# Kernel tuning notes

Measured on AMD Instinct MI355X. Metric: run time of the kernel, lower is better.

## Reference

```python
import jax, jax.numpy as jnp
from jax import lax
import numpy as np

D_MODEL = 1024
D_STATE = 16
D_CONV = 4
EXPAND = 2
D_INNER = EXPAND * D_MODEL
IN_DIM = 256
OUT_DIM = 256
B = 2
T = 1024
LN_EPS = 1e-5


def setup_inputs() -> dict:
    key = jax.random.key(0)
    ks = jax.random.split(key, 10)
    s = lambda k, shape: (jax.random.normal(k, shape, dtype=jnp.float32) * 0.02)
    inp = {}
    inp["x"] = jax.random.normal(ks[0], (B, T, IN_DIM), dtype=jnp.float32)
    inp["hidden_state"] = jnp.zeros((B, D_INNER, D_STATE), dtype=jnp.float32)
    # wrapper input projection (Linear with bias)
    inp["W_in_wrap"] = s(ks[1], (IN_DIM, D_MODEL))
    inp["b_in_wrap"] = jnp.zeros((D_MODEL,), jnp.float32)
    # LayerNorm
    inp["ln_gamma"] = jnp.ones((D_MODEL,), jnp.float32)
    inp["ln_beta"] = jnp.zeros((D_MODEL,), jnp.float32)
    # Mamba block params
    inp["W_in"] = s(ks[2], (D_MODEL, 2 * D_INNER))          # in_proj, no bias
    inp["conv_w"] = s(ks[3], (D_INNER, 1, D_CONV))           # depthwise conv kernel (O,I/G,K)
    inp["conv_b"] = jnp.zeros((D_INNER,), jnp.float32)
    inp["W_x"] = s(ks[4], (D_INNER, 2 * D_STATE + D_INNER))  # x_proj, no bias
    inp["W_dt"] = s(ks[5], (D_INNER, D_INNER))
    inp["b_dt"] = jnp.zeros((D_INNER,), jnp.float32)
    A = jnp.tile(jnp.arange(1, D_STATE + 1, dtype=jnp.float32)[None, :], (D_INNER, 1))
    inp["A_log"] = jnp.log(A)
    inp["D_skip"] = jnp.ones((D_INNER,), jnp.float32)
    inp["W_out"] = s(ks[6], (D_INNER, D_MODEL))              # out_proj, no bias
    # wrapper output projection (Linear with bias)
    inp["W_out_wrap"] = s(ks[7], (D_MODEL, OUT_DIM))
    inp["b_out_wrap"] = jnp.zeros((OUT_DIM,), jnp.float32)
    return inp


def _silu(x):
    return x * jax.nn.sigmoid(x)


def _layernorm(x, gamma, beta):
    mu = jnp.mean(x, axis=-1, keepdims=True)
    var = jnp.mean(jnp.square(x - mu), axis=-1, keepdims=True)
    return (x - mu) * lax.rsqrt(var + LN_EPS) * gamma + beta


def _mamba_forward(x, hidden_state, W_in_wrap, b_in_wrap, ln_gamma, ln_beta,
                   W_in, conv_w, conv_b, W_x, W_dt, b_dt, A_log, D_skip,
                   W_out, W_out_wrap, b_out_wrap):
    # wrapper: input projection + layernorm
    h = x @ W_in_wrap + b_in_wrap            # [B,T,d_model]
    h = _layernorm(h, ln_gamma, ln_beta)

    # Mamba block
    xz = h @ W_in                             # [B,T,2*d_inner]
    x_branch, z = jnp.split(xz, 2, axis=-1)

    # causal depthwise conv1d (torch pads both sides by d_conv-1, slices to seq_len == left-pad only)
    xc = lax.conv_general_dilated(
        x_branch.transpose(0, 2, 1),          # [B, d_inner, T]
        conv_w,                               # [d_inner, 1, K]
        window_strides=(1,),
        padding=[(D_CONV - 1, 0)],
        feature_group_count=D_INNER,
        dimension_numbers=('NCH', 'OIH', 'NCH'))
    xc = xc + conv_b[None, :, None]
    u = _silu(xc.transpose(0, 2, 1))          # [B,T,d_inner]

    proj = u @ W_x                            # [B,T,2n+d_inner]
    B_in = proj[..., :D_STATE]                # [B,T,n]
    C_in = proj[..., D_STATE:2 * D_STATE]     # [B,T,n]
    dt = jax.nn.softplus(proj[..., 2 * D_STATE:] @ W_dt + b_dt)  # [B,T,d_inner]

    A = -jnp.exp(A_log)                       # [d_inner,n]
    dA = jnp.exp(dt[..., None] * A)                              # [B,T,d,n]
    dBu = dt[..., None] * B_in[:, :, None, :] * u[..., None]     # [B,T,d,n]

    def step(h_c, inputs):
        dA_t, dBu_t, C_t = inputs             # [B,d,n],[B,d,n],[B,n]
        h_c = dA_t * h_c + dBu_t
        y_t = jnp.einsum('bdn,bn->bd', h_c, C_t)
        return h_c, y_t

    hT, ys = lax.scan(step, hidden_state,
                      (dA.transpose(1, 0, 2, 3), dBu.transpose(1, 0, 2, 3), C_in.transpose(1, 0, 2)))
    y = ys.transpose(1, 0, 2)                 # [B,T,d_inner]
    y = y + u * D_skip
    y = y * _silu(z)
    out = (y @ W_out) @ W_out_wrap + b_out_wrap
    return out, hT


def reference(x, hidden_state, W_in_wrap, b_in_wrap, ln_gamma, ln_beta,
              W_in, conv_w, conv_b, W_x, W_dt, b_dt, A_log, D_skip,
              W_out, W_out_wrap, b_out_wrap):
    return _mamba_forward(x, hidden_state, W_in_wrap, b_in_wrap, ln_gamma, ln_beta,
                          W_in, conv_w, conv_b, W_x, W_dt, b_dt, A_log, D_skip,
                          W_out, W_out_wrap, b_out_wrap)
```

## Files before the change

kernel.cpp:

```cpp
#include <hip/hip_runtime.h>
#include <cstddef>
#include <cstdint>

#define D_MODEL 1024
#define D_STATE 16
#define D_CONV 4
#define D_INNER 2048
#define IN_DIM 256
#define OUT_DIM 256
#define BATCH 2
#define SEQ 1024
#define NTOK (BATCH*SEQ)
#define PROJ_N (2*D_STATE + D_INNER)
#define CHUNK 64
#define NCHUNK (SEQ/CHUNK)

typedef __attribute__((ext_vector_type(8))) short bf16x8;
typedef __attribute__((ext_vector_type(4))) float f32x4;

__device__ __forceinline__ float siluf(float x){ return x / (1.f + __expf(-x)); }

__device__ __forceinline__ unsigned short f2bf(float f) {
  uint32_t x = __float_as_uint(f);
  uint32_t r = x + 0x7fffu + ((x >> 16) & 1u);
  return (unsigned short)(r >> 16);
}
__device__ __forceinline__ float bf2f(unsigned short u) {
  return __uint_as_float(((uint32_t)u) << 16);
}

template<int k, typename T, int N>
__device__ __forceinline__ T (&pick4(T (&a)[N], T (&b)[N], T (&c)[N], T (&d)[N]))[N] {
  if constexpr (k == 0) return a; else if constexpr (k == 1) return b;
  else if constexpr (k == 2) return c; else return d;
}

__device__ __forceinline__ void tc_tile(float (*tile)[33], const float* __restrict__ in,
                                        unsigned short* __restrict__ out,
                                        int R, int C, int tcx, int tcy, int tid)
{
  const int bc = tcx * 32, br = tcy * 32;
  const int tx = tid & 31, ty = tid >> 5;
  #pragma unroll
  for (int i = 0; i < 4; ++i) {
    int r = ty + i*8;
    tile[r][tx] = in[(size_t)(br + r)*C + bc + tx];
  }
  __syncthreads();
  const int otx = tid & 7, oty = tid >> 3;
  ushort4 v;
  v.x = f2bf(tile[otx*4+0][oty]);
  v.y = f2bf(tile[otx*4+1][oty]);
  v.z = f2bf(tile[otx*4+2][oty]);
  v.w = f2bf(tile[otx*4+3][oty]);
  *(ushort4*)&out[(size_t)(bc + oty)*R + br + otx*4] = v;
}

__global__ __launch_bounds__(256)
void prep_k(const float* __restrict__ x, const float* __restrict__ Wiw,
            const float* __restrict__ Win, const float* __restrict__ Wx,
            const float* __restrict__ Wdt, const float* __restrict__ Wout,
            const float* __restrict__ Wwr,
            unsigned short* __restrict__ xb16, unsigned short* __restrict__ WiwT,
            unsigned short* __restrict__ WinT, unsigned short* __restrict__ WxT,
            unsigned short* __restrict__ WdtT, unsigned short* __restrict__ Wob,
            unsigned short* __restrict__ WwrT)
{
  __shared__ float tile[32][33];
  const int tid = threadIdx.x;
  int id = blockIdx.x;
  if (id < 4096)  { tc_tile(tile, Win,  WinT,  1024, 4096, id % 128, id / 128, tid); return; }
  id -= 4096;
  if (id < 4160)  { tc_tile(tile, Wx,   WxT,   2048, 2080, id % 65,  id / 65,  tid); return; }
  id -= 4160;
  if (id < 4096)  { tc_tile(tile, Wdt,  WdtT,  2048, 2048, id % 64,  id / 64,  tid); return; }
  id -= 4096;
  if (id < 2048) {
    int i = id * 256 + tid;
    float4 v = ((const float4*)Wout)[i];
    ushort4 o;
    o.x = f2bf(v.x); o.y = f2bf(v.y); o.z = f2bf(v.z); o.w = f2bf(v.w);
    ((ushort4*)Wob)[i] = o;
    return;
  }
  id -= 2048;
  if (id < 256)   { tc_tile(tile, Wwr,  WwrT,  1024, 256,  id % 8,   id / 8,   tid); return; }
  id -= 256;
  if (id < 256)   { tc_tile(tile, Wiw,  WiwT,  256,  1024, id % 32,  id / 32,  tid); return; }
  id -= 256;
  if (id < 512) {
    int i = id * 256 + tid;
    float4 v = ((const float4*)x)[i];
    ushort4 o;
    o.x = f2bf(v.x); o.y = f2bf(v.y); o.z = f2bf(v.z); o.w = f2bf(v.w);
    ((ushort4*)xb16)[i] = o;
    return;
  }
  id -= 512;
  {
    unsigned short* p = WxT + (size_t)(2080 + id) * 2048 + tid * 8;
    ushort4 z = {0,0,0,0};
    *(ushort4*)p = z; *(ushort4*)(p + 4) = z;
  }
}

template<int BM, int BN, int MODE>
__global__ __launch_bounds__(256)
void gemm_bf16(const unsigned short* __restrict__ A, const unsigned short* __restrict__ B,
               int M, int N, int K, int lda, int ldb,
               const float* __restrict__ bias,
               void* __restrict__ out0, void* __restrict__ out1)
{
  constexpr int FM = BM / 32;
  constexpr int FN = BN / 32;
  constexpr int ROWS = BM + BN;
  constexpr int GR = ROWS / 64;
  __shared__ __align__(1024) unsigned short S[2][ROWS*32];

  const int tid = threadIdx.x;
  const int lane = tid & 63, w = tid >> 6;
  const int row0 = blockIdx.y * BM, col0 = blockIdx.x * BN;
  const int wr = (w >> 1) * (BM/2), wc = (w & 1) * (BN/2);
  const int l15 = lane & 15, lg4 = lane >> 4;

  size_t zoff = 0;
  if constexpr (MODE == 5) {
    A += (size_t)blockIdx.z * (size_t)K;
    B += (size_t)blockIdx.z * (size_t)K;
    zoff = (size_t)blockIdx.z * (size_t)(gridDim.y * BM) * (size_t)N;
  }

  int afo[FM], bfo[FN];
  #pragma unroll
  for (int fi = 0; fi < FM; ++fi) {
    const int r = wr + fi*16 + l15;
    afo[fi] = r*32 + (lg4 ^ ((r >> 1) & 3))*8;
  }
  #pragma unroll
  for (int fj = 0; fj < FN; ++fj) {
    const int r = wc + fj*16 + l15;
    bfo[fj] = (BM + r)*32 + (lg4 ^ ((r >> 1) & 3))*8;
  }

  const unsigned short* src[GR];
  int ldso[GR];
  #pragma unroll
  for (int i = 0; i < GR; ++i) {
    const int g = tid + i*256;
    const int row = g >> 2, q = g & 3;
    ldso[i] = row*32 + (q ^ ((row >> 1) & 3))*8;
    src[i] = (row < BM) ? A + (size_t)(row0 + row) * lda + q*8
                        : B + (size_t)(col0 + row - BM) * ldb + q*8;
  }

  f32x4 acc[FM][FN];
  #pragma unroll
  for (int i=0;i<FM;i++)
    #pragma unroll
    for (int j=0;j<FN;j++) acc[i][j] = (f32x4){0.f,0.f,0.f,0.f};

  const int NT = K >> 5;
  bf16x8 g0[GR], g1[GR], g2[GR], g3[GR];

  auto loadg = [&](bf16x8 (&g)[GR]) {
    #pragma unroll
    for (int i = 0; i < GR; ++i) { g[i] = *(const bf16x8*)src[i]; src[i] += 32; }
  };

  loadg(g0); loadg(g1); loadg(g2); loadg(g3);
  #pragma unroll
  for (int i = 0; i < GR; ++i) *(bf16x8*)(&S[0][ldso[i]]) = g0[i];
  asm volatile("s_waitcnt lgkmcnt(0)" ::: "memory");
  __builtin_amdgcn_s_barrier();
  asm volatile("" ::: "memory");

#define STEP(I) do {                                                          \
    const int j = base + (I);                                                 \
    if (j < NT) {                                                             \
      bf16x8 af[FM], bfv[FN];                                                 \
      _Pragma("unroll")                                                       \
      for (int fi = 0; fi < FM; ++fi)                                         \
        af[fi] = *(const bf16x8*)&S[(I)&1][afo[fi]];                          \
      _Pragma("unroll")                                                       \
      for (int fj = 0; fj < FN; ++fj)                                         \
        bfv[fj] = *(const bf16x8*)&S[(I)&1][bfo[fj]];                         \
      if (j + 4 < NT) loadg(pick4<(I)&3>(g0, g1, g2, g3));                    \
      _Pragma("unroll")                                                       \
      for (int fi = 0; fi < FM; ++fi)                                         \
        _Pragma("unroll")                                                     \
        for (int fj = 0; fj < FN; ++fj)                                       \
          acc[fi][fj] = __builtin_amdgcn_mfma_f32_16x16x32_bf16(              \
              af[fi], bfv[fj], acc[fi][fj], 0, 0, 0);                         \
      if (j + 1 < NT) {                                                       \
        bf16x8 (&gw)[GR] = pick4<((I)+1)&3>(g0, g1, g2, g3);                  \
        _Pragma("unroll")                                                     \
        for (int i = 0; i < GR; ++i)                                          \
          *(bf16x8*)(&S[((I)+1)&1][ldso[i]]) = gw[i];                         \
      }                                                                       \
      asm volatile("s_waitcnt lgkmcnt(0)" ::: "memory");                      \
      __builtin_amdgcn_s_barrier();                                           \
      asm volatile("" ::: "memory");                                          \
    }                                                                         \
  } while (0)

  for (int base = 0; base < NT; base += 4) {
    STEP(0); STEP(1); STEP(2); STEP(3);
  }
#undef STEP

  #pragma unroll
  for (int fi=0; fi<FM; fi++){
    const int rb = row0 + wr + fi*16 + lg4*4;
    #pragma unroll
    for (int fj=0; fj<FN; fj++){
      const int c = col0 + wc + fj*16 + l15;
      #pragma unroll
      for (int q=0;q<4;q++){
        const int r = rb + q;
        float v = acc[fi][fj][q];
        if constexpr (MODE == 0) {
          if (c < N) ((float*)out0)[(size_t)r*N + c] = bias ? v + bias[c] : v;
        } else if constexpr (MODE == 1) {
          if (c < N) { v += bias[c]; v = (v > 20.f) ? v : log1pf(__expf(v));
                       ((float*)out0)[(size_t)r*N + c] = v; }
        } else if constexpr (MODE == 2) {
          if (c < N) ((unsigned short*)out0)[(size_t)r*N + c] = f2bf(v);
        } else if constexpr (MODE == 3) {
          if (c < 2048) ((float*)out0)[(size_t)r*2048 + c] = v;
          else          ((unsigned short*)out1)[(size_t)r*2048 + (c - 2048)] = f2bf(v);
        } else if constexpr (MODE == 4) {
          if (c < 32) ((float*)out0)[(size_t)r*32 + c] = v;
          else if (c < N) ((unsigned short*)out1)[(size_t)r*2048 + (c - 32)] = f2bf(v);
        } else {
          if (c < N) ((float*)out0)[zoff + (size_t)r*N + c] = v;
        }
      }
    }
  }
}

__global__ __launch_bounds__(256)
void red4_wf(const float* __restrict__ p, unsigned short* __restrict__ out)
{
  const size_t S = (size_t)256*2048;
  const int i = (blockIdx.x * 256 + threadIdx.x) * 4;
  float4 a = *(const float4*)(p + i);
  float4 b = *(const float4*)(p + S + i);
  float4 c = *(const float4*)(p + 2*S + i);
  float4 d = *(const float4*)(p + 3*S + i);
  ushort4 o;
  o.x = f2bf(a.x+b.x+c.x+d.x);
  o.y = f2bf(a.y+b.y+c.y+d.y);
  o.z = f2bf(a.z+b.z+c.z+d.z);
  o.w = f2bf(a.w+b.w+c.w+d.w);
  *(ushort4*)(out + i) = o;
}

__global__ __launch_bounds__(256)
void red4_out(const float* __restrict__ p, const float* __restrict__ bias,
              float* __restrict__ out)
{
  const size_t S = (size_t)2048*256;
  const int i = (blockIdx.x * 256 + threadIdx.x) * 4;
  float4 a = *(const float4*)(p + i);
  float4 b = *(const float4*)(p + S + i);
  float4 c = *(const float4*)(p + 2*S + i);
  float4 d = *(const float4*)(p + 3*S + i);
  float4 bb = *(const float4*)(bias + (i & 255));
  float4 o;
  o.x = a.x+b.x+c.x+d.x + bb.x;
  o.y = a.y+b.y+c.y+d.y + bb.y;
  o.z = a.z+b.z+c.z+d.z + bb.z;
  o.w = a.w+b.w+c.w+d.w + bb.w;
  *(float4*)(out + i) = o;
}

__global__ __launch_bounds__(256)
void ln_k(const float* __restrict__ h, const float* __restrict__ gamma,
          const float* __restrict__ beta, unsigned short* __restrict__ hb)
{
  const int row = blockIdx.x;
  const float* p = h + (size_t)row * D_MODEL;
  float s = 0.f, s2 = 0.f;
  for (int i = threadIdx.x; i < D_MODEL; i += 256) { float v = p[i]; s += v; s2 += v*v; }
  #pragma unroll
  for (int off = 32; off; off >>= 1) { s += __shfl_down(s, off, 64); s2 += __shfl_down(s2, off, 64); }
  __shared__ float ss[4], ss2[4];
  __shared__ float smu, sinv;
  const int wid = threadIdx.x >> 6;
  if ((threadIdx.x & 63) == 0) { ss[wid] = s; ss2[wid] = s2; }
  __syncthreads();
  if (threadIdx.x == 0) {
    float S = ss[0]+ss[1]+ss[2]+ss[3];
    float S2 = ss2[0]+ss2[1]+ss2[2]+ss2[3];
    float mu = S * (1.f / D_MODEL);
    float var = S2 * (1.f / D_MODEL) - mu * mu;
    smu = mu; sinv = rsqrtf(var + 1e-5f);
  }
  __syncthreads();
  const float mu = smu, inv = sinv;
  unsigned short* q = hb + (size_t)row * D_MODEL;
  for (int i = threadIdx.x; i < D_MODEL; i += 256)
    q[i] = f2bf((p[i] - mu) * inv * gamma[i] + beta[i]);
}

__global__ __launch_bounds__(256)
void conv_silu_k(const float* __restrict__ xb, const float* __restrict__ cw,
                 const float* __restrict__ cb, unsigned short* __restrict__ ub)
{
  const int idx = blockIdx.x * 256 + threadIdx.x;
  const int d  = idx & (D_INNER - 1);
  const int bt = idx >> 11;
  const int t  = bt & (SEQ - 1);
  float acc = cb[d];
  const float* base = xb + (size_t)bt * D_INNER + d;
  #pragma unroll
  for (int k = 0; k < D_CONV; ++k) {
    int tt = t + k - (D_CONV - 1);
    if (tt >= 0) acc = fmaf(cw[d*D_CONV + k], base[(ptrdiff_t)(k - (D_CONV-1)) * D_INNER], acc);
  }
  ub[idx] = f2bf(siluf(acc));
}

__global__ __launch_bounds__(256)
void scan_p1(const float* __restrict__ dtb, const unsigned short* __restrict__ ub,
             const float* __restrict__ BC, const float* __restrict__ A_log,
             float* __restrict__ summ)
{
  const int bid = blockIdx.x;
  const int b = bid >> 7;
  const int c = (bid >> 3) & (NCHUNK - 1);
  const int d = ((bid & 7) << 8) + threadIdx.x;
  float A[D_STATE], hl[D_STATE];
  #pragma unroll
  for (int n = 0; n < D_STATE; ++n) { A[n] = -__expf(A_log[d*D_STATE + n]); hl[n] = 0.f; }
  float dtsum = 0.f;
  const size_t row0 = (size_t)b * SEQ + (size_t)c * CHUNK;
  float dtv = dtb[row0*D_INNER + d];
  float uv  = bf2f(ub[row0*D_INNER + d]);
  float Bv[D_STATE];
  #pragma unroll
  for (int n = 0; n < D_STATE; ++n) Bv[n] = BC[row0*32 + n];
  for (int t = 0; t < CHUNK; ++t) {
    const size_t rn = row0 + ((t+1 < CHUNK) ? (t+1) : t);
    float ndt = dtb[rn*D_INNER + d];
    float nu  = bf2f(ub[rn*D_INNER + d]);
    float nB[D_STATE];
    #pragma unroll
    for (int n = 0; n < D_STATE; ++n) nB[n] = BC[rn*32 + n];
    const float du = dtv * uv;
    dtsum += dtv;
    #pragma unroll
    for (int n = 0; n < D_STATE; ++n) {
      float dA = __expf(dtv * A[n]);
      hl[n] = fmaf(dA, hl[n], du * Bv[n]);
    }
    dtv = ndt; uv = nu;
    #pragma unroll
    for (int n = 0; n < D_STATE; ++n) Bv[n] = nB[n];
  }
  float* s = summ + (((size_t)b*NCHUNK + c)*32)*D_INNER + d;
  #pragma unroll
  for (int n = 0; n < D_STATE; ++n) {
    s[(size_t)n*D_INNER]      = __expf(A[n] * dtsum);
    s[(size_t)(16+n)*D_INNER] = hl[n];
  }
}

__global__ __launch_bounds__(256)
void scan_p2(float* __restrict__ summ, const float* __restrict__ h0,
             float* __restrict__ outH)
{
  const int b = blockIdx.x >> 3;
  const int d = ((blockIdx.x & 7) << 8) + threadIdx.x;
  float h[D_STATE];
  #pragma unroll
  for (int n = 0; n < D_STATE; ++n) h[n] = h0[((size_t)b*D_INNER + d)*D_STATE + n];
  float pv[D_STATE], lv[D_STATE];
  float* s0 = summ + (((size_t)b*NCHUNK + 0)*32)*D_INNER + d;
  #pragma unroll
  for (int n = 0; n < D_STATE; ++n) { pv[n] = s0[(size_t)n*D_INNER]; lv[n] = s0[(size_t)(16+n)*D_INNER]; }
  for (int c = 0; c < NCHUNK; ++c) {
    float* s = summ + (((size_t)b*NCHUNK + c)*32)*D_INNER + d;
    const int cn = (c+1 < NCHUNK) ? (c+1) : c;
    float* sn = summ + (((size_t)b*NCHUNK + cn)*32)*D_INNER + d;
    float np[D_STATE], nl[D_STATE];
    #pragma unroll
    for (int n = 0; n < D_STATE; ++n) { np[n] = sn[(size_t)n*D_INNER]; nl[n] = sn[(size_t)(16+n)*D_INNER]; }
    #pragma unroll
    for (int n = 0; n < D_STATE; ++n) {
      s[(size_t)n*D_INNER] = h[n];
      h[n] = fmaf(pv[n], h[n], lv[n]);
      pv[n] = np[n]; lv[n] = nl[n];
    }
  }
  #pragma unroll
  for (int n = 0; n < D_STATE; ++n)
    outH[((size_t)b*D_INNER + d)*D_STATE + n] = h[n];
}

__global__ __launch_bounds__(256)
void scan_p3(const float* __restrict__ dtb, const unsigned short* __restrict__ ub,
             const unsigned short* __restrict__ zbh, const float* __restrict__ BC,
             const float* __restrict__ A_log, const float* __restrict__ D_skip,
             const float* __restrict__ summ, unsigned short* __restrict__ yb)
{
  const int bid = blockIdx.x;
  const int b = bid >> 7;
  const int c = (bid >> 3) & (NCHUNK - 1);
  const int d = ((bid & 7) << 8) + threadIdx.x;
  float A[D_STATE], h[D_STATE];
  const float* s = summ + (((size_t)b*NCHUNK + c)*32)*D_INNER + d;
  #pragma unroll
  for (int n = 0; n < D_STATE; ++n) {
    A[n] = -__expf(A_log[d*D_STATE + n]);
    h[n] = s[(size_t)n*D_INNER];
  }
  const float Ds = D_skip[d];
  const size_t row0 = (size_t)b * SEQ + (size_t)c * CHUNK;
  float dtv = dtb[row0*D_INNER + d];
  float uv  = bf2f(ub[row0*D_INNER + d]);
  float zv  = bf2f(zbh[row0*D_INNER + d]);
  float Bv[D_STATE], Cv[D_STATE];
  #pragma unroll
  for (int n = 0; n < D_STATE; ++n) { Bv[n] = BC[row0*32 + n]; Cv[n] = BC[row0*32 + 16 + n]; }
  for (int t = 0; t < CHUNK; ++t) {
    const size_t r = row0 + t;
    const size_t rn = row0 + ((t+1 < CHUNK) ? (t+1) : t);
    float ndt = dtb[rn*D_INNER + d];
    float nu  = bf2f(ub[rn*D_INNER + d]);
    float nz  = bf2f(zbh[rn*D_INNER + d]);
    float nB[D_STATE], nC[D_STATE];
    #pragma unroll
    for (int n = 0; n < D_STATE; ++n) { nB[n] = BC[rn*32 + n]; nC[n] = BC[rn*32 + 16 + n]; }
    const float du = dtv * uv;
    float y = 0.f;
    #pragma unroll
    for (int n = 0; n < D_STATE; ++n) {
      float dA = __expf(dtv * A[n]);
      h[n] = fmaf(dA, h[n], du * Bv[n]);
      y = fmaf(h[n], Cv[n], y);
    }
    y = fmaf(uv, Ds, y);
    yb[r*D_INNER + d] = f2bf(y * siluf(zv));
    dtv = ndt; uv = nu; zv = nz;
    #pragma unroll
    for (int n = 0; n < D_STATE; ++n) { Bv[n] = nB[n]; Cv[n] = nC[n]; }
  }
}

extern "C" void kernel_launch(void* const* d_in, const int* in_sizes, int n_in,
                              void* d_out, int out_size, void* d_ws, size_t ws_size,
                              hipStream_t stream) {
  const float* x          = (const float*)d_in[0];
  const float* h0         = (const float*)d_in[1];
  const float* W_in_wrap  = (const float*)d_in[2];
  const float* b_in_wrap  = (const float*)d_in[3];
  const float* ln_g       = (const float*)d_in[4];
  const float* ln_b       = (const float*)d_in[5];
  const float* W_in       = (const float*)d_in[6];
  const float* conv_w     = (const float*)d_in[7];
  const float* conv_b     = (const float*)d_in[8];
  const float* W_x        = (const float*)d_in[9];
  const float* W_dt       = (const float*)d_in[10];
  const float* b_dt       = (const float*)d_in[11];
  const float* A_log      = (const float*)d_in[12];
  const float* D_skip     = (const float*)d_in[13];
  const float* W_out      = (const float*)d_in[14];
  const float* W_out_wrap = (const float*)d_in[15];
  const float* b_out_wrap = (const float*)d_in[16];

  float* out  = (float*)d_out;
  float* outH = out + (size_t)NTOK * OUT_DIM;

  char* ws = (char*)d_ws;
  auto at = [&](size_t kb){ return (void*)(ws + kb*1024); };
  float*          hbuf = (float*)at(0);
  float*          wfp  = hbuf;
  float*          summ = hbuf;
  float*          xb   = (float*)at(8192);
  float*          dtb  = xb;
  float*          outp = xb;
  unsigned short* zbh  = (unsigned short*)at(24576);
  unsigned short* WfT  = (unsigned short*)at(32768);
  unsigned short* ub   = (unsigned short*)at(40960);
  unsigned short* xb16 = ub;
  unsigned short* gb   = (unsigned short*)at(49152);
  unsigned short* WiwT = gb;
  unsigned short* yb   = gb;
  unsigned short* hb   = (unsigned short*)at(57344);
  float*          BC   = (float*)at(61440);
  unsigned short* WinT = (unsigned short*)at(61696);
  unsigned short* WxT  = (unsigned short*)at(69888);
  unsigned short* WdtT = (unsigned short*)at(78592);
  unsigned short* Wob  = (unsigned short*)at(86784);
  unsigned short* WwrT = (unsigned short*)at(90880);

  dim3 blk(256);
  prep_k<<<dim3(15520), blk, 0, stream>>>(x, W_in_wrap, W_in, W_x, W_dt, W_out, W_out_wrap,
                                          xb16, WiwT, WinT, WxT, WdtT, Wob, WwrT);
  gemm_bf16<64,64,5><<<dim3(2048/64, 256/64, 4), blk, 0, stream>>>(WwrT, Wob, 256, 2048, 1024/4,
                                                                   1024, 1024, nullptr, wfp, nullptr);
  red4_wf<<<dim3(512), blk, 0, stream>>>(wfp, WfT);
  gemm_bf16<64,64,0><<<dim3(1024/64, NTOK/64), blk, 0, stream>>>(xb16, WiwT, NTOK, 1024, 256,
                                                                 256, 256, b_in_wrap, hbuf, nullptr);
  ln_k<<<dim3(NTOK), blk, 0, stream>>>(hbuf, ln_g, ln_b, hb);
  gemm_bf16<128,64,3><<<dim3(4096/64, NTOK/128), blk, 0, stream>>>(hb, WinT, NTOK, 4096, 1024,
                                                                   1024, 1024, nullptr, xb, zbh);
  conv_silu_k<<<dim3(NTOK*D_INNER/256), blk, 0, stream>>>(xb, conv_w, conv_b, ub);
  gemm_bf16<128,64,4><<<dim3(2112/64, NTOK/128), blk, 0, stream>>>(ub, WxT, NTOK, PROJ_N, 2048,
                                                                   2048, 2048, nullptr, BC, gb);
  gemm_bf16<128,64,1><<<dim3(2048/64, NTOK/128), blk, 0, stream>>>(gb, WdtT, NTOK, 2048, 2048,
                                                                   2048, 2048, b_dt, dtb, nullptr);
  scan_p1<<<dim3(BATCH*NCHUNK*(D_INNER/256)), blk, 0, stream>>>(dtb, ub, BC, A_log, summ);
  scan_p2<<<dim3(BATCH*(D_INNER/256)), blk, 0, stream>>>(summ, h0, outH);
  scan_p3<<<dim3(BATCH*NCHUNK*(D_INNER/256)), blk, 0, stream>>>(dtb, ub, zbh, BC, A_log, D_skip, summ, yb);
  gemm_bf16<64,64,5><<<dim3(256/64, NTOK/64, 4), blk, 0, stream>>>(yb, WfT, NTOK, 256, 2048/4,
                                                                   2048, 2048, nullptr, outp, nullptr);
  red4_out<<<dim3(512), blk, 0, stream>>>(outp, b_out_wrap, out);
}
```

Baseline: 296.5 us.

## Add 128x128 direct-to-LDS double-buffered GEMM for the three main projections

Adds a new 512-thread bf16 MFMA GEMM kernel with 128x128 output tiles and a K step of 64. It loads global memory straight into LDS with global_load_lds, uses an XOR-swizzled layout to avoid bank conflicts, double-buffers across K steps and raises wave priority around the MFMA bursts. It replaces the older 128x64 kernel for in_proj, x_proj and dt_proj, keeping the same epilogues. The larger tiles give more reuse per load and less register staging, in exchange for 64KB of LDS per block, which lowers occupancy. The x_proj grid now reads padding rows up to 2176; those columns are masked out on store.

New measurement: 265.6 us. 1.12x faster.

```diff
diff --git a/kernel.cpp b/kernel.cpp
--- a/kernel.cpp
+++ b/kernel.cpp
@@ -27,6 +27,11 @@
 }
 __device__ __forceinline__ float bf2f(unsigned short u) {
   return __uint_as_float(((uint32_t)u) << 16);
+}
+
+__device__ __forceinline__ void gload16(const void* g, void* l) {
+  __builtin_amdgcn_global_load_lds((const __attribute__((address_space(1))) void*)g,
+                                   (__attribute__((address_space(3))) void*)l, 16, 0, 0);
 }
 
 template<int k, typename T, int N>
@@ -101,6 +106,117 @@
     unsigned short* p = WxT + (size_t)(2080 + id) * 2048 + tid * 8;
     ushort4 z = {0,0,0,0};
     *(ushort4*)p = z; *(ushort4*)(p + 4) = z;
+  }
+}
+
+template<int MODE>
+__global__ __launch_bounds__(512)
+void gemm2ph(const unsigned short* __restrict__ A, const unsigned short* __restrict__ B,
+             int M, int N, int K, int lda, int ldb,
+             const float* __restrict__ bias,
+             void* __restrict__ out0, void* __restrict__ out1)
+{
+  __shared__ __align__(1024) unsigned short S[2][256*64];
+  const int tid = threadIdx.x;
+  const int lane = tid & 63, w = tid >> 6;
+  const int row0 = blockIdx.y * 128, col0 = blockIdx.x * 128;
+  const int wr = (w >> 2) * 64, wc = (w & 3) * 32;
+  const int l15 = lane & 15, lg4 = lane >> 4;
+
+  int afo[4][2], bfo[2][2];
+  #pragma unroll
+  for (int fi = 0; fi < 4; ++fi)
+    #pragma unroll
+    for (int h = 0; h < 2; ++h) {
+      const int r = wr + fi*16 + l15;
+      const int q = h*4 + lg4;
+      afo[fi][h] = r*64 + (q ^ (r & 7))*8;
+    }
+  #pragma unroll
+  for (int fj = 0; fj < 2; ++fj)
+    #pragma unroll
+    for (int h = 0; h < 2; ++h) {
+      const int r = wc + fj*16 + l15;
+      const int q = h*4 + lg4;
+      bfo[fj][h] = (128 + r)*64 + (q ^ (r & 7))*8;
+    }
+
+  const unsigned short* src[4];
+  int dsto[4];
+  #pragma unroll
+  for (int i = 0; i < 4; ++i) {
+    const int base = w*32 + i*8;
+    const int row = base + (lane >> 3);
+    const int gs = (lane & 7) ^ (row & 7);
+    dsto[i] = base*64;
+    src[i] = (row < 128) ? A + (size_t)(row0 + row) * lda + gs*8
+                         : B + (size_t)(col0 + row - 128) * ldb + gs*8;
+  }
+
+  f32x4 acc[4][2];
+  #pragma unroll
+  for (int i=0;i<4;i++)
+    #pragma unroll
+    for (int j=0;j<2;j++) acc[i][j] = (f32x4){0.f,0.f,0.f,0.f};
+
+  const int NT = K >> 6;
+
+  auto stage = [&](int buf) {
+    #pragma unroll
+    for (int i = 0; i < 4; ++i) { gload16(src[i], &S[buf][dsto[i]]); src[i] += 64; }
+  };
+
+  stage(0);
+  asm volatile("s_waitcnt vmcnt(0)" ::: "memory");
+  __builtin_amdgcn_s_barrier();
+  asm volatile("" ::: "memory");
+
+  int cur = 0;
+  for (int t = 0; t < NT; ++t) {
+    if (t + 1 < NT) stage(cur ^ 1);
+    #pragma unroll
+    for (int h = 0; h < 2; ++h) {
+      bf16x8 af[4], bfv[2];
+      #pragma unroll
+      for (int fi = 0; fi < 4; ++fi) af[fi] = *(const bf16x8*)&S[cur][afo[fi][h]];
+      #pragma unroll
+      for (int fj = 0; fj < 2; ++fj) bfv[fj] = *(const bf16x8*)&S[cur][bfo[fj][h]];
+      __builtin_amdgcn_s_setprio(1);
+      #pragma unroll
+      for (int fi = 0; fi < 4; ++fi)
+        #pragma unroll
+        for (int fj = 0; fj < 2; ++fj)
+          acc[fi][fj] = __builtin_amdgcn_mfma_f32_16x16x32_bf16(af[fi], bfv[fj], acc[fi][fj], 0, 0, 0);
+      __builtin_amdgcn_s_setprio(0);
+    }
+    asm volatile("s_waitcnt vmcnt(0) lgkmcnt(0)" ::: "memory");
+    __builtin_amdgcn_s_barrier();
+    asm volatile("" ::: "memory");
+    cur ^= 1;
+  }
+
+  #pragma unroll
+  for (int fi=0; fi<4; fi++){
+    const int rb = row0 + wr + fi*16 + lg4*4;
+    #pragma unroll
+    for (int fj=0; fj<2; fj++){
+      const int c = col0 + wc + fj*16 + l15;
+      #pragma unroll
+      for (int q=0;q<4;q++){
+        const int r = rb + q;
+        float v = acc[fi][fj][q];
+        if constexpr (MODE == 1) {
+          if (c < N) { v += bias[c]; v = (v > 20.f) ? v : log1pf(__expf(v));
+                       ((float*)out0)[(size_t)r*N + c] = v; }
+        } else if constexpr (MODE == 3) {
+          if (c < 2048) ((float*)out0)[(size_t)r*2048 + c] = v;
+          else          ((unsigned short*)out1)[(size_t)r*2048 + (c - 2048)] = f2bf(v);
+        } else {
+          if (c < 32) ((float*)out0)[(size_t)r*32 + c] = v;
+          else if (c < N) ((unsigned short*)out1)[(size_t)r*2048 + (c - 32)] = f2bf(v);
+        }
+      }
+    }
   }
 }
 
@@ -220,17 +336,8 @@
         float v = acc[fi][fj][q];
         if constexpr (MODE == 0) {
           if (c < N) ((float*)out0)[(size_t)r*N + c] = bias ? v + bias[c] : v;
-        } else if constexpr (MODE == 1) {
-          if (c < N) { v += bias[c]; v = (v > 20.f) ? v : log1pf(__expf(v));
-                       ((float*)out0)[(size_t)r*N + c] = v; }
         } else if constexpr (MODE == 2) {
           if (c < N) ((unsigned short*)out0)[(size_t)r*N + c] = f2bf(v);
-        } else if constexpr (MODE == 3) {
-          if (c < 2048) ((float*)out0)[(size_t)r*2048 + c] = v;
-          else          ((unsigned short*)out1)[(size_t)r*2048 + (c - 2048)] = f2bf(v);
-        } else if constexpr (MODE == 4) {
-          if (c < 32) ((float*)out0)[(size_t)r*32 + c] = v;
-          else if (c < N) ((unsigned short*)out1)[(size_t)r*2048 + (c - 32)] = f2bf(v);
         } else {
           if (c < N) ((float*)out0)[zoff + (size_t)r*N + c] = v;
         }
@@ -497,6 +604,7 @@
   unsigned short* WwrT = (unsigned short*)at(90880);
 
   dim3 blk(256);
+  dim3 blk512(512);
   prep_k<<<dim3(15520), blk, 0, stream>>>(x, W_in_wrap, W_in, W_x, W_dt, W_out, W_out_wrap,
                                           xb16, WiwT, WinT, WxT, WdtT, Wob, WwrT);
   gemm_bf16<64,64,5><<<dim3(2048/64, 256/64, 4), blk, 0, stream>>>(WwrT, Wob, 256, 2048, 1024/4,
@@ -505,13 +613,13 @@
   gemm_bf16<64,64,0><<<dim3(1024/64, NTOK/64), blk, 0, stream>>>(xb16, WiwT, NTOK, 1024, 256,
                                                                  256, 256, b_in_wrap, hbuf, nullptr);
   ln_k<<<dim3(NTOK), blk, 0, stream>>>(hbuf, ln_g, ln_b, hb);
-  gemm_bf16<128,64,3><<<dim3(4096/64, NTOK/128), blk, 0, stream>>>(hb, WinT, NTOK, 4096, 1024,
-                                                                   1024, 1024, nullptr, xb, zbh);
+  gemm2ph<3><<<dim3(4096/128, NTOK/128), blk512, 0, stream>>>(hb, WinT, NTOK, 4096, 1024,
+                                                              1024, 1024, nullptr, xb, zbh);
   conv_silu_k<<<dim3(NTOK*D_INNER/256), blk, 0, stream>>>(xb, conv_w, conv_b, ub);
-  gemm_bf16<128,64,4><<<dim3(2112/64, NTOK/128), blk, 0, stream>>>(ub, WxT, NTOK, PROJ_N, 2048,
-                                                                   2048, 2048, nullptr, BC, gb);
-  gemm_bf16<128,64,1><<<dim3(2048/64, NTOK/128), blk, 0, stream>>>(gb, WdtT, NTOK, 2048, 2048,
-                                                                   2048, 2048, b_dt, dtb, nullptr);
+  gemm2ph<4><<<dim3(2176/128, NTOK/128), blk512, 0, stream>>>(ub, WxT, NTOK, PROJ_N, 2048,
+                                                              2048, 2048, nullptr, BC, gb);
+  gemm2ph<1><<<dim3(2048/128, NTOK/128), blk512, 0, stream>>>(gb, WdtT, NTOK, 2048, 2048,
+                                                              2048, 2048, b_dt, dtb, nullptr);
   scan_p1<<<dim3(BATCH*NCHUNK*(D_INNER/256)), blk, 0, stream>>>(dtb, ub, BC, A_log, summ);
   scan_p2<<<dim3(BATCH*(D_INNER/256)), blk, 0, stream>>>(summ, h0, outH);
   scan_p3<<<dim3(BATCH*NCHUNK*(D_INNER/256)), blk, 0, stream>>>(dtb, ub, zbh, BC, A_log, D_skip, summ, yb);
```
